# Kernel tuning notes

Measured on AMD Instinct MI355X. Metric: run time of the kernel, lower is better.

## Reference

```python
import jax, jax.numpy as jnp
import numpy as np

N, E = 25000, 400000
IN, HID, OUT = 128, 256, 128
T = 4                      # towers
F1, F2 = HID // T, OUT // T  # per-tower out dims (divide_input=False)
A = 12                     # len(aggregators)=4 * len(scalers)=3
EPS_STD = 1e-5
EPS_BN = 1e-5


def _glorot(k, shape):
    fin, fout = shape[-2], shape[-1]
    lim = float(np.sqrt(6.0 / (fin + fout)))
    return jax.random.uniform(k, shape, jnp.float32, -lim, lim)


def setup_inputs():
    key = jax.random.key(0)
    ks = jax.random.split(key, 10)
    x = jax.random.normal(ks[0], (N, IN), jnp.float32)
    edge_index = jax.random.randint(ks[1], (2, E), 0, N, dtype=jnp.int32)
    # avg_deg['log'] buffer of PNAConv: mean over nodes of log(deg+1)
    deg = jax.ops.segment_sum(jnp.ones((E,), jnp.float32), edge_index[1], num_segments=N)
    avg_log = jnp.mean(jnp.log(deg + 1.0)).astype(jnp.float32)
    return dict(
        x=x, edge_index=edge_index, avg_log=avg_log,
        pre1_W=_glorot(ks[2], (T, 2 * IN, F1)), pre1_b=jnp.zeros((T, F1), jnp.float32),
        post1_W=_glorot(ks[3], (T, IN + A * F1, F1)), post1_b=jnp.zeros((T, F1), jnp.float32),
        lin1_W=_glorot(ks[4], (T * F1, HID)), lin1_b=jnp.zeros((HID,), jnp.float32),
        bn1_g=jnp.ones((HID,), jnp.float32), bn1_b=jnp.zeros((HID,), jnp.float32),
        pre2_W=_glorot(ks[5], (T, 2 * HID, F2)), pre2_b=jnp.zeros((T, F2), jnp.float32),
        post2_W=_glorot(ks[6], (T, HID + A * F2, F2)), post2_b=jnp.zeros((T, F2), jnp.float32),
        lin2_W=_glorot(ks[7], (T * F2, OUT)), lin2_b=jnp.zeros((OUT,), jnp.float32),
        bn2_g=jnp.ones((OUT,), jnp.float32), bn2_b=jnp.zeros((OUT,), jnp.float32),
    )


def _pna(x, src, tgt, preW, preB, postW, postB, linW, linB, avg_log):
    """PNAConv: towers=T, divide_input=False, pre_layers=post_layers=1,
    aggregators [mean,min,max,std], scalers [identity,amplification,attenuation]."""
    n = x.shape[0]
    # message: per tower Linear on concat([x_i, x_j]) where i=target, j=source
    h = jnp.concatenate([x[tgt], x[src]], axis=-1)            # [E, 2*F_in]
    msg = jnp.einsum('ec,tcf->etf', h, preW) + preB           # [E, T, F]
    ones = jnp.ones((msg.shape[0],), msg.dtype)
    deg = jax.ops.segment_sum(ones, tgt, num_segments=n)      # in-degree [n]
    degc = jnp.maximum(deg, 1.0)[:, None, None]
    s1 = jax.ops.segment_sum(msg, tgt, num_segments=n)
    mean = s1 / degc
    s2 = jax.ops.segment_sum(msg * msg, tgt, num_segments=n)
    var = jnp.maximum(s2 / degc - mean * mean, 0.0)
    std = jnp.sqrt(var + EPS_STD)
    has = (deg > 0.0)[:, None, None]
    mn = jnp.where(has, jax.ops.segment_min(msg, tgt, num_segments=n), 0.0)
    mx = jnp.where(has, jax.ops.segment_max(msg, tgt, num_segments=n), 0.0)
    agg = jnp.concatenate([mean, mn, mx, std], axis=-1)       # [n, T, 4F]
    dlog = jnp.log(jnp.maximum(deg, 1.0) + 1.0)[:, None, None]
    out = jnp.concatenate([agg, agg * (dlog / avg_log), agg * (avg_log / dlog)], axis=-1)  # [n, T, 12F]
    xt = jnp.broadcast_to(x[:, None, :], (n, T, x.shape[-1]))
    post_in = jnp.concatenate([xt, out], axis=-1)             # [n, T, F_in + 12F]
    post = jnp.einsum('ntc,tcf->ntf', post_in, postW) + postB # [n, T, F]
    return post.reshape(n, -1) @ linW + linB                  # [n, out]


def _bn(x, g, b):
    # BatchNorm1d training-mode math: biased batch variance
    m = jnp.mean(x, axis=0)
    v = jnp.mean((x - m) ** 2, axis=0)
    return g * (x - m) / jnp.sqrt(v + EPS_BN) + b


def reference(x, edge_index, avg_log, pre1_W, pre1_b, post1_W, post1_b, lin1_W, lin1_b,
              bn1_g, bn1_b, pre2_W, pre2_b, post2_W, post2_b, lin2_W, lin2_b, bn2_g, bn2_b):
    src, tgt = edge_index[0], edge_index[1]
    h = _pna(x, src, tgt, pre1_W, pre1_b, post1_W, post1_b, lin1_W, lin1_b, avg_log)
    h = jax.nn.relu(_bn(jnp.nan_to_num(h), bn1_g, bn1_b))
    h = _pna(h, src, tgt, pre2_W, pre2_b, post2_W, post2_b, lin2_W, lin2_b, avg_log)
    h = jax.nn.relu(_bn(jnp.nan_to_num(h), bn2_g, bn2_b))
    return h
```

## Files before the change

### kernel.cpp

```cpp
#include <hip/hip_runtime.h>
#include <hip/hip_bf16.h>
#include <float.h>
#include <math.h>

typedef __hip_bfloat16 bf16;
typedef __attribute__((ext_vector_type(8))) short short8;
typedef __attribute__((ext_vector_type(4))) float f32x4;

__device__ __forceinline__ float bf2f(bf16 v){ return __bfloat162float(v); }
__device__ __forceinline__ void stv(float* p, float v){ *p = v; }
__device__ __forceinline__ void stv(bf16* p, float v){ *p = __float2bfloat16(v); }
__device__ __forceinline__ float nanfix(float v){
  if (v != v) return 0.f;
  return fminf(fmaxf(v, -FLT_MAX), FLT_MAX);
}
__device__ __forceinline__ unsigned short f2bu(float f){
  unsigned u = __float_as_uint(f);
  unsigned r = u + 0x7FFFu + ((u>>16)&1u);
  return (unsigned short)(r>>16);
}
template<int VEC>
__device__ __forceinline__ void ldbf(const bf16* p, float (&o)[VEC]){
  if constexpr (VEC==4){
    ushort4 r = *(const ushort4*)p;
    o[0]=__uint_as_float((unsigned)r.x<<16); o[1]=__uint_as_float((unsigned)r.y<<16);
    o[2]=__uint_as_float((unsigned)r.z<<16); o[3]=__uint_as_float((unsigned)r.w<<16);
  } else {
    ushort2 r = *(const ushort2*)p;
    o[0]=__uint_as_float((unsigned)r.x<<16); o[1]=__uint_as_float((unsigned)r.y<<16);
  }
}

__global__ void k_deg(const int* __restrict__ tgt, int* __restrict__ deg, int E){
  int e = blockIdx.x*blockDim.x + threadIdx.x;
  if (e < E) atomicAdd(&deg[tgt[e]], 1);
}

__global__ void k_scan1(const int* __restrict__ deg, int* __restrict__ bsum, int N){
  __shared__ int sm[256];
  int i = blockIdx.x*256 + threadIdx.x;
  sm[threadIdx.x] = (i < N) ? deg[i] : 0;
  __syncthreads();
  for (int off = 128; off > 0; off >>= 1){
    if (threadIdx.x < off) sm[threadIdx.x] += sm[threadIdx.x + off];
    __syncthreads();
  }
  if (threadIdx.x == 0) bsum[blockIdx.x] = sm[0];
}

__global__ void k_scan2(int* __restrict__ bsum, int NB){
  __shared__ int sm[1024];
  int tid = threadIdx.x;
  sm[tid] = (tid < NB) ? bsum[tid] : 0;
  __syncthreads();
  for (int off = 1; off < 1024; off <<= 1){
    int t = (tid >= off) ? sm[tid-off] : 0;
    __syncthreads();
    sm[tid] += t;
    __syncthreads();
  }
  if (tid < NB) bsum[tid] = (tid == 0) ? 0 : sm[tid-1];
}

__global__ void k_scan3(const int* __restrict__ deg, const int* __restrict__ bsum,
                        int* __restrict__ offs, int N){
  __shared__ int sm[256];
  int tid = threadIdx.x;
  int i = blockIdx.x*256 + tid;
  int v = (i < N) ? deg[i] : 0;
  sm[tid] = v; __syncthreads();
  for (int off = 1; off < 256; off <<= 1){
    int t = (tid >= off) ? sm[tid-off] : 0;
    __syncthreads();
    sm[tid] += t;
    __syncthreads();
  }
  if (i < N) offs[i+1] = bsum[blockIdx.x] + sm[tid];
  if (i == 0) offs[0] = 0;
}

__global__ void k_scatter(const int* __restrict__ src, const int* __restrict__ tgt,
                          const int* __restrict__ offs, int* __restrict__ cnt,
                          int* __restrict__ ssrc, int E){
  int e = blockIdx.x*blockDim.x + threadIdx.x;
  if (e < E){
    int t = tgt[e];
    int pos = offs[t] + atomicAdd(&cnt[t], 1);
    ssrc[pos] = src[e];
  }
}

__device__ __forceinline__ void rp_pqT(const float* preW, const float* preB,
                                       bf16* WpqT, float* bpq, int K, int F, int idx){
  int NC = 4*F;
  int total = 2*NC*K;
  if (idx < total){
    int j = idx/K, c = idx%K;
    int half = j/NC, jj = j%NC, t = jj/F, f = jj%F;
    WpqT[idx] = __float2bfloat16(preW[(t*2*K + half*K + c)*F + f]);
  }
  if (idx < 2*NC) bpq[idx] = (idx < NC) ? preB[idx] : 0.f;
}
__device__ __forceinline__ void rp_xT(const float* postW, const float* postB,
                                      bf16* WxT, float* bpost, int KX, int F, int idx){
  int NC = 4*F; int KP = KX + 12*F;
  if (idx < NC*KX){
    int j = idx/KX, c = idx%KX, t = j/F, f = j%F;
    WxT[idx] = __float2bfloat16(postW[(t*KP + c)*F + f]);
  }
  if (idx < NC) bpost[idx] = postB[idx];
}
__device__ __forceinline__ void rp_agg3(const float* postW, bf16* Wagg3,
                                        int KX, int F, int idx){
  int K4F = 4*F; int KP = KX + 12*F;
  int total = 4*3*F*K4F;
  if (idx < total){
    int k = idx % K4F; int r = idx / K4F;
    int zr = r % (3*F); int t = r / (3*F);
    int s = zr / F, f = zr % F;
    Wagg3[idx] = __float2bfloat16(postW[((size_t)(t*KP + KX + s*K4F + k))*F + f]);
  }
}
__device__ __forceinline__ void rp_linT(const float* linW, bf16* WlinT,
                                        int K, int NC, int idx){
  if (idx < NC*K){
    int j = idx/K, c = idx%K;
    WlinT[idx] = __float2bfloat16(linW[c*NC + j]);
  }
}

struct SetupArgs {
  const float *pre1W, *pre1b, *post1W, *post1b, *lin1W;
  const float *pre2W, *pre2b, *post2W, *post2b, *lin2W;
  const float *x;
  bf16 *WpqT1, *WxT1, *Wagg31, *lin1WT;
  bf16 *WpqT2, *WxT2, *Wagg32, *lin2WT;
  bf16 *x_bf;
  float *bpq1, *bpost1, *bpq2, *bpost2;
  int nx4;
  int gstride;
};

__global__ void k_setup(SetupArgs a){
  int idx = blockIdx.x*256 + threadIdx.x;
  switch (blockIdx.y){
    case 0: rp_pqT (a.pre1W, a.pre1b, a.WpqT1, a.bpq1, 128, 64, idx); break;
    case 1: rp_xT  (a.post1W, a.post1b, a.WxT1, a.bpost1, 128, 64, idx); break;
    case 2: rp_agg3(a.post1W, a.Wagg31, 128, 64, idx); break;
    case 3: rp_linT(a.lin1W, a.lin1WT, 256, 256, idx); break;
    case 4: rp_pqT (a.pre2W, a.pre2b, a.WpqT2, a.bpq2, 256, 32, idx); break;
    case 5: rp_xT  (a.post2W, a.post2b, a.WxT2, a.bpost2, 256, 32, idx); break;
    case 6: rp_agg3(a.post2W, a.Wagg32, 256, 32, idx); break;
    case 7: rp_linT(a.lin2W, a.lin2WT, 128, 128, idx); break;
    case 8:
      for (int i = idx; i < a.nx4; i += a.gstride){
        float4 v = *(const float4*)(a.x + (size_t)i*4);
        ushort4 o = make_ushort4(f2bu(v.x), f2bu(v.y), f2bu(v.z), f2bu(v.w));
        *(ushort4*)(a.x_bf + (size_t)i*4) = o;
      }
      break;
  }
}

template<typename TO>
__global__ __launch_bounds__(256) void k_mgemm(
    const bf16* __restrict__ A, int lda,
    const bf16* __restrict__ Bt,
    const float* __restrict__ bias,
    TO* __restrict__ Cout, int ldc,
    int N, int K, int NC)
{
  __shared__ __align__(16) bf16 As[64*40];
  __shared__ __align__(16) bf16 Bs[64*40];
  int n0 = blockIdx.y*64;
  int j0 = blockIdx.x*64;
  int tid = threadIdx.x;
  int srow = tid>>2, skoff = (tid&3)*8;
  int wave = tid>>6, lane = tid&63;
  int wy = (wave>>1)*32, wx = (wave&1)*32;
  int l15 = lane&15, q = lane>>4;
  f32x4 acc[2][2] = {};
  for (int k0 = 0; k0 < K; k0 += 32){
    uint4 av = {0,0,0,0};
    int ar = n0 + srow;
    if (ar < N) av = *(const uint4*)(A + (size_t)ar*lda + k0 + skoff);
    *(uint4*)&As[srow*40 + skoff] = av;
    uint4 bv = {0,0,0,0};
    int br = j0 + srow;
    if (br < NC) bv = *(const uint4*)(Bt + (size_t)br*K + k0 + skoff);
    *(uint4*)&Bs[srow*40 + skoff] = bv;
    __syncthreads();
    short8 af[2], bfr[2];
    #pragma unroll
    for (int i = 0; i < 2; i++){
      af[i]  = *(const short8*)&As[(wy + i*16 + l15)*40 + q*8];
      bfr[i] = *(const short8*)&Bs[(wx + i*16 + l15)*40 + q*8];
    }
    #pragma unroll
    for (int mi = 0; mi < 2; mi++)
      #pragma unroll
      for (int ni = 0; ni < 2; ni++)
        acc[mi][ni] = __builtin_amdgcn_mfma_f32_16x16x32_bf16(af[mi], bfr[ni], acc[mi][ni], 0, 0, 0);
    __syncthreads();
  }
  #pragma unroll
  for (int mi = 0; mi < 2; mi++){
    #pragma unroll
    for (int ni = 0; ni < 2; ni++){
      #pragma unroll
      for (int r = 0; r < 4; r++){
        int n  = n0 + wy + mi*16 + q*4 + r;
        int jj = j0 + wx + ni*16 + l15;
        if (n < N && jj < NC){
          float v = acc[mi][ni][r] + bias[jj];
          stv(&Cout[(size_t)n*ldc + jj], v);
        }
      }
    }
  }
}

template<int COLS, int KX>
__global__ __launch_bounds__(256) void k_postx(
    const bf16* __restrict__ X,
    const bf16* __restrict__ agg,
    const bf16* __restrict__ WxT,
    const bf16* __restrict__ Wagg3,
    const float* __restrict__ bias,
    const float* __restrict__ scal,
    bf16* __restrict__ Cout, int ldc, int N)
{
  constexpr int K4F = 4*COLS;
  constexpr int ROWS3 = 3*COLS;
  constexpr int NI = COLS/32;
  constexpr int LDA_AGG = 16*COLS;
  __shared__ __align__(16) bf16 As[64*40];
  __shared__ __align__(16) bf16 Bs[ROWS3*40];
  int z = blockIdx.z;
  int n0 = blockIdx.y*64;
  int tid = threadIdx.x;
  int srow = tid>>2, skoff = (tid&3)*8;
  int wave = tid>>6, lane = tid&63;
  int wy = (wave>>1)*32;
  int wx = (wave&1)*(COLS/2);
  int l15 = lane&15, q = lane>>4;
  f32x4 accx[2][NI] = {};
  f32x4 acc[2][NI][3] = {};
  const bf16* Bx = WxT + (size_t)z*COLS*KX;
  for (int k0 = 0; k0 < KX; k0 += 32){
    uint4 av = {0,0,0,0};
    int ar = n0 + srow;
    if (ar < N) av = *(const uint4*)(X + (size_t)ar*KX + k0 + skoff);
    *(uint4*)&As[srow*40 + skoff] = av;
    if (srow < COLS){
      uint4 bv = *(const uint4*)(Bx + (size_t)srow*KX + k0 + skoff);
      *(uint4*)&Bs[srow*40 + skoff] = bv;
    }
    __syncthreads();
    short8 af[2];
    #pragma unroll
    for (int i = 0; i < 2; i++)
      af[i] = *(const short8*)&As[(wy + i*16 + l15)*40 + q*8];
    #pragma unroll
    for (int ni = 0; ni < NI; ni++){
      short8 bfr = *(const short8*)&Bs[(wx + ni*16 + l15)*40 + q*8];
      #pragma unroll
      for (int mi = 0; mi < 2; mi++)
        accx[mi][ni] = __builtin_amdgcn_mfma_f32_16x16x32_bf16(af[mi], bfr, accx[mi][ni], 0, 0, 0);
    }
    __syncthreads();
  }
  const bf16* Az = agg + (size_t)z*K4F;
  const bf16* Bz = Wagg3 + (size_t)z*ROWS3*K4F;
  for (int k0 = 0; k0 < K4F; k0 += 32){
    uint4 av = {0,0,0,0};
    int ar = n0 + srow;
    if (ar < N) av = *(const uint4*)(Az + (size_t)ar*LDA_AGG + k0 + skoff);
    *(uint4*)&As[srow*40 + skoff] = av;
    for (int r = srow; r < ROWS3; r += 64){
      uint4 bv = *(const uint4*)(Bz + (size_t)r*K4F + k0 + skoff);
      *(uint4*)&Bs[r*40 + skoff] = bv;
    }
    __syncthreads();
    short8 af[2];
    #pragma unroll
    for (int i = 0; i < 2; i++)
      af[i] = *(const short8*)&As[(wy + i*16 + l15)*40 + q*8];
    #pragma unroll
    for (int s = 0; s < 3; s++){
      #pragma unroll
      for (int ni = 0; ni < NI; ni++){
        short8 bfr = *(const short8*)&Bs[(s*COLS + wx + ni*16 + l15)*40 + q*8];
        #pragma unroll
        for (int mi = 0; mi < 2; mi++)
          acc[mi][ni][s] = __builtin_amdgcn_mfma_f32_16x16x32_bf16(af[mi], bfr, acc[mi][ni][s], 0, 0, 0);
      }
    }
    __syncthreads();
  }
  #pragma unroll
  for (int mi = 0; mi < 2; mi++){
    #pragma unroll
    for (int ni = 0; ni < NI; ni++){
      int jj = wx + ni*16 + l15;
      int jg = z*COLS + jj;
      float bj = bias[jg];
      #pragma unroll
      for (int r = 0; r < 4; r++){
        int n = n0 + wy + mi*16 + q*4 + r;
        if (n < N){
          float s1 = scal[2*n], s2 = scal[2*n+1];
          float v = bj + accx[mi][ni][r]
                  + acc[mi][ni][0][r] + s1*acc[mi][ni][1][r] + s2*acc[mi][ni][2][r];
          Cout[(size_t)n*ldc + jg] = __float2bfloat16(v);
        }
      }
    }
  }
}

template<int NC, int F>
__global__ __launch_bounds__(256) void k_agg(const bf16* __restrict__ PQ,
    const int* __restrict__ ssrc, const int* __restrict__ offs,
    const float* __restrict__ avgp,
    bf16* __restrict__ agg, float* __restrict__ scal, int N){
  constexpr int VEC = NC/64;
  int wave = threadIdx.x>>6, lane = threadIdx.x&63;
  int n = blockIdx.x*4 + wave;
  if (n >= N) return;
  int c0 = lane*VEC;
  float p[VEC];
  ldbf<VEC>(PQ + (size_t)n*2*NC + c0, p);
  int s0 = offs[n], s1 = offs[n+1];
  float sum[VEC], sq[VEC], mn[VEC], mx[VEC];
  #pragma unroll
  for (int v=0;v<VEC;v++){ sum[v]=0.f; sq[v]=0.f; mn[v]=FLT_MAX; mx[v]=-FLT_MAX; }
  const bf16* Q = PQ + NC + c0;
  int i = s0;
  for (; i+7 < s1; i += 8){
    int se[8];
    #pragma unroll
    for (int u=0;u<8;u++) se[u] = ssrc[i+u];
    float qv[8][VEC];
    #pragma unroll
    for (int u=0;u<8;u++) ldbf<VEC>(Q + (size_t)se[u]*2*NC, qv[u]);
    #pragma unroll
    for (int u=0;u<8;u++){
      #pragma unroll
      for (int v=0;v<VEC;v++){
        float m = p[v]+qv[u][v];
        sum[v] += m; sq[v] = fmaf(m,m,sq[v]);
        mn[v] = fminf(mn[v], m); mx[v] = fmaxf(mx[v], m);
      }
    }
  }
  for (; i+3 < s1; i += 4){
    int se[4];
    #pragma unroll
    for (int u=0;u<4;u++) se[u] = ssrc[i+u];
    float qv[4][VEC];
    #pragma unroll
    for (int u=0;u<4;u++) ldbf<VEC>(Q + (size_t)se[u]*2*NC, qv[u]);
    #pragma unroll
    for (int u=0;u<4;u++){
      #pragma unroll
      for (int v=0;v<VEC;v++){
        float m = p[v]+qv[u][v];
        sum[v] += m; sq[v] = fmaf(m,m,sq[v]);
        mn[v] = fminf(mn[v], m); mx[v] = fmaxf(mx[v], m);
      }
    }
  }
  for (; i < s1; i++){
    int sa = ssrc[i];
    float qa[VEC];
    ldbf<VEC>(Q + (size_t)sa*2*NC, qa);
    #pragma unroll
    for (int v=0;v<VEC;v++){
      float m = p[v]+qa[v];
      sum[v]+=m; sq[v]=fmaf(m,m,sq[v]); mn[v]=fminf(mn[v],m); mx[v]=fmaxf(mx[v],m);
    }
  }
  int deg = s1-s0;
  float degc = fmaxf((float)deg, 1.f);
  unsigned short um[VEC], un[VEC], ux[VEC], us[VEC];
  #pragma unroll
  for (int v=0;v<VEC;v++){
    float mean = sum[v]/degc;
    float var = fmaxf(sq[v]/degc - mean*mean, 0.f);
    float sd = sqrtf(var + 1e-5f);
    float mnv = deg>0 ? mn[v] : 0.f;
    float mxv = deg>0 ? mx[v] : 0.f;
    um[v]=f2bu(mean); un[v]=f2bu(mnv); ux[v]=f2bu(mxv); us[v]=f2bu(sd);
  }
  int t = c0 / F, f0 = c0 % F;
  bf16* base = agg + (size_t)n*4*NC + (size_t)t*4*F + f0;
  if constexpr (VEC==4){
    *(ushort4*)(base)       = make_ushort4(um[0],um[1],um[2],um[3]);
    *(ushort4*)(base + F)   = make_ushort4(un[0],un[1],un[2],un[3]);
    *(ushort4*)(base + 2*F) = make_ushort4(ux[0],ux[1],ux[2],ux[3]);
    *(ushort4*)(base + 3*F) = make_ushort4(us[0],us[1],us[2],us[3]);
  } else {
    *(ushort2*)(base)       = make_ushort2(um[0],um[1]);
    *(ushort2*)(base + F)   = make_ushort2(un[0],un[1]);
    *(ushort2*)(base + 2*F) = make_ushort2(ux[0],ux[1]);
    *(ushort2*)(base + 3*F) = make_ushort2(us[0],us[1]);
  }
  if (lane==0){
    float dlog = logf(degc + 1.f);
    float avg = *avgp;
    scal[2*n]   = dlog/avg;
    scal[2*n+1] = avg/dlog;
  }
}

template<int C>
__global__ __launch_bounds__(256) void k_bn_part(const float* __restrict__ h,
                                                 float* __restrict__ part, int N){
  constexpr int C4 = C/4;
  constexpr int RG = 256/C4;
  constexpr int RPB = 128;
  int c4 = threadIdx.x % C4, rg = threadIdx.x / C4;
  int n0 = blockIdx.x*RPB;
  int n1 = min(n0 + RPB, N);
  float4 s = {0,0,0,0}, q = {0,0,0,0};
  for (int n = n0 + rg; n < n1; n += RG){
    float4 v = *(const float4*)(h + (size_t)n*C + c4*4);
    v.x = nanfix(v.x); v.y = nanfix(v.y); v.z = nanfix(v.z); v.w = nanfix(v.w);
    s.x += v.x; s.y += v.y; s.z += v.z; s.w += v.w;
    q.x += v.x*v.x; q.y += v.y*v.y; q.z += v.z*v.z; q.w += v.w*v.w;
  }
  __shared__ float4 ssum[256], ssq[256];
  ssum[threadIdx.x] = s; ssq[threadIdx.x] = q;
  __syncthreads();
  if (rg == 0){
    #pragma unroll
    for (int g = 1; g < RG; g++){
      float4 o = ssum[g*C4 + c4];
      s.x += o.x; s.y += o.y; s.z += o.z; s.w += o.w;
      float4 p = ssq[g*C4 + c4];
      q.x += p.x; q.y += p.y; q.z += p.z; q.w += p.w;
    }
    float* dst = part + (size_t)blockIdx.x*2*C;
    *(float4*)(dst + c4*4)     = s;
    *(float4*)(dst + C + c4*4) = q;
  }
}

template<int C>
__global__ __launch_bounds__(256) void k_bn_final(const float* __restrict__ part, int PB,
                                                  float* __restrict__ stats){
  int c = blockIdx.x*256 + threadIdx.x;
  if (c >= 2*C) return;
  int CH = gridDim.y;
  int per = (PB + CH - 1)/CH;
  int p0 = blockIdx.y*per, p1 = min(p0 + per, PB);
  float acc = 0.f;
  int p = p0;
  for (; p+4 <= p1; p += 4){
    acc += part[(size_t)p*2*C + c] + part[(size_t)(p+1)*2*C + c]
         + part[(size_t)(p+2)*2*C + c] + part[(size_t)(p+3)*2*C + c];
  }
  for (; p < p1; p++) acc += part[(size_t)p*2*C + c];
  atomicAdd(&stats[c], acc);
}

template<typename TO, int C>
__global__ void k_bn_apply(const float* __restrict__ h, const float* __restrict__ stats,
     const float* __restrict__ g, const float* __restrict__ b,
     TO* __restrict__ out, int N){
  int idx = blockIdx.x*blockDim.x + threadIdx.x;
  if (idx >= N*(C/4)) return;
  int c = (idx % (C/4))*4;
  float fn = (float)N;
  float4 v = *(const float4*)(h + (size_t)idx*4);
  float r[4];
  #pragma unroll
  for (int k = 0; k < 4; k++){
    float m = stats[c+k]/fn;
    float var = fmaxf(stats[C+c+k]/fn - m*m, 0.f);
    float inv = rsqrtf(var + 1e-5f);
    float vv = nanfix(((const float*)&v)[k]);
    r[k] = fmaxf(g[c+k]*(vv - m)*inv + b[c+k], 0.f);
  }
  if constexpr (sizeof(TO) == 4){
    float4 o = {r[0], r[1], r[2], r[3]};
    *(float4*)((float*)out + (size_t)idx*4) = o;
  } else {
    ushort4 o = make_ushort4(f2bu(r[0]), f2bu(r[1]), f2bu(r[2]), f2bu(r[3]));
    *(ushort4*)((bf16*)out + (size_t)idx*4) = o;
  }
}

static inline int cdiv(int a, int b){ return (a + b - 1)/b; }

extern "C" void kernel_launch(void* const* d_in, const int* in_sizes, int n_in,
                              void* d_out, int out_size, void* d_ws, size_t ws_size,
                              hipStream_t stream){
  const int IN = 128, HID = 256, T = 4, F1 = 64, F2 = 32;
  const int N = in_sizes[0]/IN;
  const int E = in_sizes[1]/2;
  const int NC1 = T*F1;
  const int NC2 = T*F2;

  const float* x      = (const float*)d_in[0];
  const int*   ei     = (const int*)  d_in[1];
  const int*   srcE   = ei;
  const int*   tgtE   = ei + E;
  const float* avgp   = (const float*)d_in[2];
  const float* pre1W  = (const float*)d_in[3];
  const float* pre1b  = (const float*)d_in[4];
  const float* post1W = (const float*)d_in[5];
  const float* post1b = (const float*)d_in[6];
  const float* lin1W  = (const float*)d_in[7];
  const float* lin1b  = (const float*)d_in[8];
  const float* bn1g   = (const float*)d_in[9];
  const float* bn1b   = (const float*)d_in[10];
  const float* pre2W  = (const float*)d_in[11];
  const float* pre2b  = (const float*)d_in[12];
  const float* post2W = (const float*)d_in[13];
  const float* post2b = (const float*)d_in[14];
  const float* lin2W  = (const float*)d_in[15];
  const float* lin2b  = (const float*)d_in[16];
  const float* bn2g   = (const float*)d_in[17];
  const float* bn2b   = (const float*)d_in[18];

  char* w = (char*)d_ws;
  auto alloc = [&](size_t bytes)->void*{
    void* p = (void*)w; w += (bytes + 255) & ~(size_t)255; return p;
  };
  bf16* WpqT1  = (bf16*)alloc((size_t)2*NC1*IN*2);    float* bpq1   = (float*)alloc(2*NC1*4);
  bf16* WxT1   = (bf16*)alloc((size_t)NC1*IN*2);      float* bpost1 = (float*)alloc(NC1*4);
  bf16* Wagg31 = (bf16*)alloc((size_t)T*3*F1*4*F1*2);
  bf16* lin1WT = (bf16*)alloc((size_t)HID*NC1*2);
  bf16* WpqT2  = (bf16*)alloc((size_t)2*NC2*HID*2);   float* bpq2   = (float*)alloc(2*NC2*4);
  bf16* WxT2   = (bf16*)alloc((size_t)NC2*HID*2);     float* bpost2 = (float*)alloc(NC2*4);
  bf16* Wagg32 = (bf16*)alloc((size_t)T*3*F2*4*F2*2);
  bf16* lin2WT = (bf16*)alloc((size_t)128*NC2*2);
  int* deg_i   = (int*)alloc((size_t)N*4);
  int* cnt     = (int*)alloc((size_t)N*4);
  float* stats = (float*)alloc(1024*4);
  size_t zbytes = (size_t)((char*)stats - (char*)deg_i) + 1024*4;
  int* offs    = (int*)alloc((size_t)(N+1)*4);
  int* bsum    = (int*)alloc((size_t)cdiv(N,256)*4);
  int* ssrc    = (int*)alloc((size_t)E*4);
  bf16* x_bf   = (bf16*)alloc((size_t)N*IN*2);
  bf16* PQ     = (bf16*)alloc((size_t)N*512*2);
  bf16* aggb   = (bf16*)alloc((size_t)N*4*NC1*2);
  float* scal  = (float*)alloc((size_t)N*2*4);
  bf16* postbb = (bf16*)alloc((size_t)N*256*2);
  float* hpre  = (float*)alloc((size_t)N*256*4);
  bf16* h1b    = (bf16*)alloc((size_t)N*256*2);
  int PB = cdiv(N,128);
  float* part  = (float*)alloc((size_t)PB*512*4);

  hipMemsetAsync(deg_i, 0, zbytes, stream);

  int sgx = cdiv(T*3*F1*4*F1, 256);
  SetupArgs sa = { pre1W, pre1b, post1W, post1b, lin1W,
                   pre2W, pre2b, post2W, post2b, lin2W,
                   x,
                   WpqT1, WxT1, Wagg31, lin1WT,
                   WpqT2, WxT2, Wagg32, lin2WT,
                   x_bf,
                   bpq1, bpost1, bpq2, bpost2,
                   N*IN/4, sgx*256 };
  k_setup<<<dim3(sgx, 9),256,0,stream>>>(sa);

  int NBs = cdiv(N,256);
  k_deg<<<cdiv(E,256),256,0,stream>>>(tgtE, deg_i, E);
  k_scan1<<<NBs,256,0,stream>>>(deg_i, bsum, N);
  k_scan2<<<1,1024,0,stream>>>(bsum, NBs);
  k_scan3<<<NBs,256,0,stream>>>(deg_i, bsum, offs, N);
  k_scatter<<<cdiv(E,256),256,0,stream>>>(srcE, tgtE, offs, cnt, ssrc, E);

  int NB = cdiv(N,64);

  k_mgemm<bf16><<<dim3(8,NB),256,0,stream>>>(x_bf, IN, WpqT1, bpq1, PQ, 512, N, IN, 512);
  k_agg<256,64><<<cdiv(N,4),256,0,stream>>>(PQ, ssrc, offs, avgp, aggb, scal, N);
  k_postx<64,128><<<dim3(1,NB,T),256,0,stream>>>(x_bf, aggb, WxT1, Wagg31, bpost1, scal,
                                                 postbb, NC1, N);
  k_mgemm<float><<<dim3(4,NB),256,0,stream>>>(postbb, NC1, lin1WT, lin1b, hpre, HID, N, NC1, HID);
  k_bn_part<256><<<PB,256,0,stream>>>(hpre, part, N);
  k_bn_final<256><<<dim3(2,4),256,0,stream>>>(part, PB, stats);
  k_bn_apply<bf16,256><<<cdiv(N*64,256),256,0,stream>>>(hpre, stats, bn1g, bn1b, h1b, N);

  k_mgemm<bf16><<<dim3(4,NB),256,0,stream>>>(h1b, HID, WpqT2, bpq2, PQ, 256, N, HID, 256);
  k_agg<128,32><<<cdiv(N,4),256,0,stream>>>(PQ, ssrc, offs, avgp, aggb, scal, N);
  k_postx<32,256><<<dim3(1,NB,T),256,0,stream>>>(h1b, aggb, WxT2, Wagg32, bpost2, scal,
                                                 postbb, NC2, N);
  k_mgemm<float><<<dim3(2,NB),256,0,stream>>>(postbb, NC2, lin2WT, lin2b, hpre, 128, N, NC2, 128);
  k_bn_part<128><<<PB,256,0,stream>>>(hpre, part, N);
  k_bn_final<128><<<dim3(1,4),256,0,stream>>>(part, PB, stats + 512);
  k_bn_apply<float,128><<<cdiv(N*32,256),256,0,stream>>>(hpre, stats + 512, bn2g, bn2b, (float*)d_out, N);
}
```

Measured before the change: 383.9 us.

## Load post-GEMM MFMA fragments directly from global memory instead of LDS

The post-aggregation GEMM kernel drops its shared-memory staging tiles and barriers. Each lane now loads its A and B MFMA fragments straight from global memory, with the k loops fully unrolled. This removes LDS traffic and __syncthreads stalls and raises occupancy through lower LDS use. In exchange, each weight fragment is fetched by several waves and relies on L1/L2 hits, and the per-lane loads are less coalesced than the old cooperative tile loads.

New measurement: 437.1 us. 13.9% more time.

```diff
diff --git a/kernel.cpp b/kernel.cpp
--- a/kernel.cpp
+++ b/kernel.cpp
@@ -234,69 +234,53 @@
   constexpr int ROWS3 = 3*COLS;
   constexpr int NI = COLS/32;
   constexpr int LDA_AGG = 16*COLS;
-  __shared__ __align__(16) bf16 As[64*40];
-  __shared__ __align__(16) bf16 Bs[ROWS3*40];
   int z = blockIdx.z;
   int n0 = blockIdx.y*64;
   int tid = threadIdx.x;
-  int srow = tid>>2, skoff = (tid&3)*8;
   int wave = tid>>6, lane = tid&63;
   int wy = (wave>>1)*32;
   int wx = (wave&1)*(COLS/2);
   int l15 = lane&15, q = lane>>4;
+  const short8 zfrag = {};
   f32x4 accx[2][NI] = {};
   f32x4 acc[2][NI][3] = {};
-  const bf16* Bx = WxT + (size_t)z*COLS*KX;
-  for (int k0 = 0; k0 < KX; k0 += 32){
-    uint4 av = {0,0,0,0};
-    int ar = n0 + srow;
-    if (ar < N) av = *(const uint4*)(X + (size_t)ar*KX + k0 + skoff);
-    *(uint4*)&As[srow*40 + skoff] = av;
-    if (srow < COLS){
-      uint4 bv = *(const uint4*)(Bx + (size_t)srow*KX + k0 + skoff);
-      *(uint4*)&Bs[srow*40 + skoff] = bv;
-    }
-    __syncthreads();
-    short8 af[2];
-    #pragma unroll
-    for (int i = 0; i < 2; i++)
-      af[i] = *(const short8*)&As[(wy + i*16 + l15)*40 + q*8];
-    #pragma unroll
-    for (int ni = 0; ni < NI; ni++){
-      short8 bfr = *(const short8*)&Bs[(wx + ni*16 + l15)*40 + q*8];
-      #pragma unroll
-      for (int mi = 0; mi < 2; mi++)
-        accx[mi][ni] = __builtin_amdgcn_mfma_f32_16x16x32_bf16(af[mi], bfr, accx[mi][ni], 0, 0, 0);
-    }
-    __syncthreads();
-  }
-  const bf16* Az = agg + (size_t)z*K4F;
-  const bf16* Bz = Wagg3 + (size_t)z*ROWS3*K4F;
-  for (int k0 = 0; k0 < K4F; k0 += 32){
-    uint4 av = {0,0,0,0};
-    int ar = n0 + srow;
-    if (ar < N) av = *(const uint4*)(Az + (size_t)ar*LDA_AGG + k0 + skoff);
-    *(uint4*)&As[srow*40 + skoff] = av;
-    for (int r = srow; r < ROWS3; r += 64){
-      uint4 bv = *(const uint4*)(Bz + (size_t)r*K4F + k0 + skoff);
-      *(uint4*)&Bs[r*40 + skoff] = bv;
-    }
-    __syncthreads();
-    short8 af[2];
-    #pragma unroll
-    for (int i = 0; i < 2; i++)
-      af[i] = *(const short8*)&As[(wy + i*16 + l15)*40 + q*8];
-    #pragma unroll
-    for (int s = 0; s < 3; s++){
+  int r0 = n0 + wy + l15;
+  int r1 = r0 + 16;
+  bool v0 = r0 < N, v1 = r1 < N;
+  {
+    const bf16* A0 = X + (size_t)(v0 ? r0 : 0)*KX + q*8;
+    const bf16* A1 = X + (size_t)(v1 ? r1 : 0)*KX + q*8;
+    const bf16* B0 = WxT + ((size_t)z*COLS + wx + l15)*KX + q*8;
+    #pragma unroll
+    for (int k0 = 0; k0 < KX; k0 += 32){
+      short8 a0 = v0 ? *(const short8*)(A0 + k0) : zfrag;
+      short8 a1 = v1 ? *(const short8*)(A1 + k0) : zfrag;
       #pragma unroll
       for (int ni = 0; ni < NI; ni++){
-        short8 bfr = *(const short8*)&Bs[(s*COLS + wx + ni*16 + l15)*40 + q*8];
+        short8 b = *(const short8*)(B0 + (size_t)ni*16*KX + k0);
+        accx[0][ni] = __builtin_amdgcn_mfma_f32_16x16x32_bf16(a0, b, accx[0][ni], 0, 0, 0);
+        accx[1][ni] = __builtin_amdgcn_mfma_f32_16x16x32_bf16(a1, b, accx[1][ni], 0, 0, 0);
+      }
+    }
+  }
+  {
+    const bf16* A0 = agg + (size_t)(v0 ? r0 : 0)*LDA_AGG + z*K4F + q*8;
+    const bf16* A1 = agg + (size_t)(v1 ? r1 : 0)*LDA_AGG + z*K4F + q*8;
+    const bf16* B0 = Wagg3 + ((size_t)z*ROWS3 + wx + l15)*K4F + q*8;
+    #pragma unroll
+    for (int k0 = 0; k0 < K4F; k0 += 32){
+      short8 a0 = v0 ? *(const short8*)(A0 + k0) : zfrag;
+      short8 a1 = v1 ? *(const short8*)(A1 + k0) : zfrag;
+      #pragma unroll
+      for (int s = 0; s < 3; s++){
         #pragma unroll
-        for (int mi = 0; mi < 2; mi++)
-          acc[mi][ni][s] = __builtin_amdgcn_mfma_f32_16x16x32_bf16(af[mi], bfr, acc[mi][ni][s], 0, 0, 0);
-      }
-    }
-    __syncthreads();
+        for (int ni = 0; ni < NI; ni++){
+          short8 b = *(const short8*)(B0 + (size_t)(s*COLS + ni*16)*K4F + k0);
+          acc[0][ni][s] = __builtin_amdgcn_mfma_f32_16x16x32_bf16(a0, b, acc[0][ni][s], 0, 0, 0);
+          acc[1][ni][s] = __builtin_amdgcn_mfma_f32_16x16x32_bf16(a1, b, acc[1][ni][s], 0, 0, 0);
+        }
+      }
+    }
   }
   #pragma unroll
   for (int mi = 0; mi < 2; mi++){
```
